# Kernel tuning notes

Measured on AMD Instinct MI355X. Metric: run time of the kernel, lower is better.

## Reference

```python
import jax, jax.numpy as jnp
import numpy as np

HIDDEN = 4096
N_HEADS = 32
N_KV_HEADS = 8
HEAD_DIM = 128
ROPE_THETA = 1e11
KEY_MULTIPLIER = 0.5
Q_SIZE = N_HEADS * HEAD_DIM
KV_SIZE = N_KV_HEADS * HEAD_DIM
SEQ = 2048


def _rope_neox(x, positions):
    # x: [T, H, D]; neox style: rotate halves of the head dim
    d = x.shape[-1]
    inv_freq = 1.0 / (ROPE_THETA ** (jnp.arange(0, d // 2, dtype=jnp.float32) * (2.0 / d)))
    freqs = positions.astype(jnp.float32)[:, None] * inv_freq[None, :]  # [T, D/2]
    cos = jnp.cos(freqs)[:, None, :]  # [T, 1, D/2]
    sin = jnp.sin(freqs)[:, None, :]
    x1, x2 = x[..., : d // 2], x[..., d // 2 :]
    return jnp.concatenate([x1 * cos - x2 * sin, x2 * cos + x1 * sin], axis=-1)


def setup_inputs() -> dict:
    key = jax.random.key(0)
    k1, k2, k3 = jax.random.split(key, 3)
    scale_in = 1.0 / np.sqrt(HIDDEN)
    return {
        "positions": jnp.arange(SEQ, dtype=jnp.int32),
        "hidden_states": jax.random.normal(k1, (SEQ, HIDDEN), jnp.float32),
        "w_qkv": jax.random.normal(k2, (HIDDEN, Q_SIZE + 2 * KV_SIZE), jnp.float32) * scale_in,
        "w_o": jax.random.normal(k3, (Q_SIZE, HIDDEN), jnp.float32) * scale_in,
    }


def reference(positions, hidden_states, w_qkv, w_o):
    T = hidden_states.shape[0]
    qkv = hidden_states @ w_qkv  # [T, q+2kv]
    q, k, v = jnp.split(qkv, [Q_SIZE, Q_SIZE + KV_SIZE], axis=-1)
    k = k * KEY_MULTIPLIER
    q = q.reshape(T, N_HEADS, HEAD_DIM)
    k = k.reshape(T, N_KV_HEADS, HEAD_DIM)
    v = v.reshape(T, N_KV_HEADS, HEAD_DIM)
    q = _rope_neox(q, positions)
    k = _rope_neox(k, positions)
    # GQA: expand kv heads to query heads
    group = N_HEADS // N_KV_HEADS
    k = jnp.repeat(k, group, axis=1)  # [T, H, D]
    v = jnp.repeat(v, group, axis=1)
    scaling = HEAD_DIM ** -0.5
    scores = jnp.einsum("qhd,khd->hqk", q, k) * scaling  # [H, T, T]
    causal = positions[:, None] >= positions[None, :]  # [T, T]
    scores = jnp.where(causal[None, :, :], scores, jnp.finfo(scores.dtype).min)
    probs = jax.nn.softmax(scores, axis=-1)
    attn = jnp.einsum("hqk,khd->qhd", probs, v).reshape(T, Q_SIZE)
    return attn @ w_o
```

## Files before the change

kernel.cpp:

```cpp
#include <hip/hip_runtime.h>
#include <hip/hip_bf16.h>
#include <math.h>

typedef __bf16 bf16_t;
typedef bf16_t bf16x8 __attribute__((ext_vector_type(8)));
typedef bf16_t bf16x4 __attribute__((ext_vector_type(4)));
typedef float  f32x4  __attribute__((ext_vector_type(4)));

#define HIDDEN 4096
#define NH     32
#define NKV    8
#define HD     128
#define QSZ    4096
#define KVSZ   1024
#define QKVN   6144
#define SEQ    2048
#define ATT_SCALE 0.08838834764831845f
#define KEYMUL 0.5f

static __device__ __forceinline__ void gld_lds16(const void* g, void* l) {
  __builtin_amdgcn_global_load_lds((const __attribute__((address_space(1))) char*)g,
                                   (__attribute__((address_space(3))) char*)l, 16, 0, 0);
}

__global__ __launch_bounds__(256) void cast_f32_bf16(const float* __restrict__ in,
                                                     bf16_t* __restrict__ out) {
  int i = (blockIdx.x * 256 + threadIdx.x) * 4;
  float4 v = *(const float4*)(in + i);
  bf16x4 o;
  o[0] = (bf16_t)v.x; o[1] = (bf16_t)v.y; o[2] = (bf16_t)v.z; o[3] = (bf16_t)v.w;
  *(bf16x4*)(out + i) = o;
}

__global__ __launch_bounds__(256) void transpose_cast(const float* __restrict__ W,
                                                      bf16_t* __restrict__ WT,
                                                      int K, int N) {
  __shared__ float t[32][33];
  int k0 = blockIdx.y * 32, n0 = blockIdx.x * 32;
  int c = threadIdx.x & 31, r = threadIdx.x >> 5;
#pragma unroll
  for (int rr = r; rr < 32; rr += 8)
    t[rr][c] = W[(size_t)(k0 + rr) * N + n0 + c];
  __syncthreads();
#pragma unroll
  for (int rr = r; rr < 32; rr += 8)
    WT[(size_t)(n0 + rr) * K + k0 + c] = (bf16_t)t[c][rr];
}

__global__ __launch_bounds__(256) void vprep(const float* __restrict__ qkv,
                                             bf16_t* __restrict__ VT) {
  __shared__ float t[32][33];
  int h = blockIdx.z;
  int s0 = blockIdx.x * 32, d0 = blockIdx.y * 32;
  int c = threadIdx.x & 31, r = threadIdx.x >> 5;
#pragma unroll
  for (int rr = r; rr < 32; rr += 8)
    t[rr][c] = qkv[(size_t)(s0 + rr) * QKVN + QSZ + KVSZ + h * HD + d0 + c];
  __syncthreads();
#pragma unroll
  for (int rr = r; rr < 32; rr += 8)
    VT[((size_t)h * HD + d0 + rr) * SEQ + s0 + c] = (bf16_t)t[c][rr];
}

__global__ __launch_bounds__(256) void rope_qk(const float* __restrict__ qkv,
                                               const int* __restrict__ positions,
                                               bf16_t* __restrict__ Qh,
                                               bf16_t* __restrict__ Kh) {
  int s = blockIdx.x;
  float pos = (float)positions[s];
  for (int p = threadIdx.x; p < (NH + NKV) * 64; p += 256) {
    int i = p & 63;
    float inv = powf(100000000000.0f, -(float)i * (1.0f / 64.0f));
    float fr = pos * inv;
    float cs = cosf(fr), sn = sinf(fr);
    if (p < NH * 64) {
      int hh = p >> 6;
      const float* base = qkv + (size_t)s * QKVN + hh * HD;
      float x1 = base[i], x2 = base[i + 64];
      bf16_t* ob = Qh + ((size_t)hh * SEQ + s) * HD;
      ob[i]      = (bf16_t)(x1 * cs - x2 * sn);
      ob[i + 64] = (bf16_t)(x2 * cs + x1 * sn);
    } else {
      int hh = (p - NH * 64) >> 6;
      const float* base = qkv + (size_t)s * QKVN + QSZ + hh * HD;
      float x1 = base[i], x2 = base[i + 64];
      bf16_t* ob = Kh + ((size_t)hh * SEQ + s) * HD;
      ob[i]      = (bf16_t)((x1 * cs - x2 * sn) * KEYMUL);
      ob[i + 64] = (bf16_t)((x2 * cs + x1 * sn) * KEYMUL);
    }
  }
}

__global__ __launch_bounds__(512, 2) void gemm256(const bf16_t* __restrict__ A,
                                                  const bf16_t* __restrict__ BT,
                                                  float* __restrict__ C,
                                                  int M, int N, int K) {
  __shared__ __align__(16) bf16_t lA[2][256 * 64];
  __shared__ __align__(16) bf16_t lB[2][256 * 64];
  const int tid = threadIdx.x;
  const int w = tid >> 6, lane = tid & 63, l16 = lane & 15, lhi = lane >> 4;
  const int wm2 = w >> 2, wn4 = w & 3;

  const int nbx = N >> 8;
  const int nwg = nbx * (M >> 8);
  int bid = blockIdx.x;
  int swz = (bid & 7) * (nwg >> 3) + (bid >> 3);
  const int bm = swz / nbx, bn = swz % nbx;

  const int NT = K >> 6;

  int sRow[4], sCol[4];
#pragma unroll
  for (int i = 0; i < 4; ++i) {
    int X = i * 8192 + tid * 16;
    sRow[i] = X >> 7;
    sCol[i] = (X & 127) ^ ((sRow[i] & 7) << 4);
  }
  const char* Ag = (const char*)(A + (size_t)bm * 256 * K);
  const char* Bg = (const char*)(BT + (size_t)bn * 256 * K);

  auto stage = [&](int t, int buf) {
#pragma unroll
    for (int i = 0; i < 4; ++i)
      gld_lds16(Ag + (size_t)sRow[i] * (K * 2) + t * 128 + sCol[i],
                (char*)&lA[buf][0] + i * 8192 + tid * 16);
#pragma unroll
    for (int i = 0; i < 4; ++i)
      gld_lds16(Bg + (size_t)sRow[i] * (K * 2) + t * 128 + sCol[i],
                (char*)&lB[buf][0] + i * 8192 + tid * 16);
  };

  f32x4 acc[8][4] = {};
  stage(0, 0);
  stage(1, 1);

  for (int t = 0; t < NT; ++t) {
    const int cur = t & 1;
    if (t == NT - 1) asm volatile("s_waitcnt vmcnt(0)" ::: "memory");
    else             asm volatile("s_waitcnt vmcnt(8)" ::: "memory");
    __builtin_amdgcn_s_barrier();
    asm volatile("" ::: "memory");
    const char* Ab = (const char*)&lA[cur][0];
    const char* Bb = (const char*)&lB[cur][0];

    bf16x8 bF[4][2];
#pragma unroll
    for (int n = 0; n < 4; ++n)
#pragma unroll
      for (int ks = 0; ks < 2; ++ks) {
        int row = wn4 * 64 + n * 16 + l16;
        bF[n][ks] = *(const bf16x8*)(Bb + row * 128 + ((ks * 64 + lhi * 16) ^ ((row & 7) << 4)));
      }
#pragma unroll
    for (int q = 0; q < 4; ++q) {
      bf16x8 aF[2][2];
#pragma unroll
      for (int mi = 0; mi < 2; ++mi)
#pragma unroll
        for (int ks = 0; ks < 2; ++ks) {
          int row = wm2 * 128 + (q * 2 + mi) * 16 + l16;
          aF[mi][ks] = *(const bf16x8*)(Ab + row * 128 + ((ks * 64 + lhi * 16) ^ ((row & 7) << 4)));
        }
      __builtin_amdgcn_s_setprio(1);
#pragma unroll
      for (int mi = 0; mi < 2; ++mi)
#pragma unroll
        for (int n = 0; n < 4; ++n)
#pragma unroll
          for (int ks = 0; ks < 2; ++ks)
            acc[q * 2 + mi][n] = __builtin_amdgcn_mfma_f32_16x16x32_bf16(
                aF[mi][ks], bF[n][ks], acc[q * 2 + mi][n], 0, 0, 0);
      __builtin_amdgcn_s_setprio(0);
    }
    asm volatile("" ::: "memory");
    __builtin_amdgcn_s_barrier();
    asm volatile("" ::: "memory");
    if (t + 2 < NT) stage(t + 2, cur);
  }

#pragma unroll
  for (int m = 0; m < 8; ++m) {
    int row = bm * 256 + wm2 * 128 + m * 16 + lhi * 4;
#pragma unroll
    for (int n = 0; n < 4; ++n) {
      int col = bn * 256 + wn4 * 64 + n * 16 + l16;
#pragma unroll
      for (int j = 0; j < 4; ++j)
        C[(size_t)(row + j) * N + col] = acc[m][n][j];
    }
  }
}

__global__ __launch_bounds__(256) void attn_kernel(const bf16_t* __restrict__ Q,
                                                   const bf16_t* __restrict__ Kb,
                                                   const bf16_t* __restrict__ VT,
                                                   bf16_t* __restrict__ Oa) {
  __shared__ __align__(16) char KV[2][2][16384];
  __shared__ __align__(16) bf16_t Plds[4][16][72];
  int h = blockIdx.y, p = blockIdx.x;
  int kvh = h >> 2;
  int tid = threadIdx.x;
  int w = tid >> 6, lane = tid & 63;
  int l16 = lane & 15, lhi = lane >> 4;
  int xr = (l16 & 7) << 4;

  int kRow[4], kCol[4], vRow[4], vCol[4], ldsOff[4];
#pragma unroll
  for (int i = 0; i < 4; ++i) {
    int X = w * 4096 + i * 1024 + lane * 16;
    ldsOff[i] = X;
    kRow[i] = X >> 8;
    kCol[i] = (X & 255) ^ ((kRow[i] & 7) << 4);
    vRow[i] = X >> 7;
    vCol[i] = (X & 127) ^ ((vRow[i] & 7) << 4);
  }
  const char* Kg = (const char*)(Kb + (size_t)kvh * SEQ * HD);
  const char* Vg = (const char*)(VT + (size_t)kvh * HD * SEQ);

  int qts[2] = {p, 31 - p};
  int nts[2] = {p + 1, 32 - p};

  for (int ph = 0; ph < 2; ++ph) {
    int qt = qts[ph], ntile = nts[ph];
    int qrow0 = qt * 64 + w * 16;

    bf16x8 qf[4];
    const bf16_t* qbase = Q + ((size_t)h * SEQ + qrow0 + l16) * HD;
#pragma unroll
    for (int kk = 0; kk < 4; ++kk)
      qf[kk] = *(const bf16x8*)(qbase + kk * 32 + lhi * 8);

    f32x4 o[8] = {};
    float m_r[4], l_r[4];
#pragma unroll
    for (int j = 0; j < 4; ++j) { m_r[j] = -1e30f; l_r[j] = 0.0f; }

#pragma unroll
    for (int i = 0; i < 4; ++i) {
      gld_lds16(Kg + (size_t)(0 + kRow[i]) * 256 + kCol[i], &KV[0][0][0] + ldsOff[i]);
      gld_lds16(Vg + (size_t)vRow[i] * (SEQ * 2) + 0 + vCol[i], &KV[0][1][0] + ldsOff[i]);
    }
    __syncthreads();

    for (int kt = 0; kt < ntile; ++kt) {
      int b = kt & 1;
      int kb = kt * 64;
      if (kt + 1 < ntile) {
        int kb2 = kb + 64;
#pragma unroll
        for (int i = 0; i < 4; ++i) {
          gld_lds16(Kg + (size_t)(kb2 + kRow[i]) * 256 + kCol[i], &KV[b ^ 1][0][0] + ldsOff[i]);
          gld_lds16(Vg + (size_t)vRow[i] * (SEQ * 2) + (size_t)kb2 * 2 + vCol[i], &KV[b ^ 1][1][0] + ldsOff[i]);
        }
      }
      const char* Kl = &KV[b][0][0];
      const char* Vl = &KV[b][1][0];

      f32x4 s4[4] = {};
#pragma unroll
      for (int n = 0; n < 4; ++n) {
        int r = n * 16 + l16;
#pragma unroll
        for (int kk = 0; kk < 4; ++kk) {
          bf16x8 kf = *(const bf16x8*)(Kl + r * 256 + ((kk * 64 + lhi * 16) ^ xr));
          s4[n] = __builtin_amdgcn_mfma_f32_16x16x32_bf16(qf[kk], kf, s4[n], 0, 0, 0);
        }
      }
      float pv[4][4];
#pragma unroll
      for (int n = 0; n < 4; ++n) {
        int col = kb + n * 16 + l16;
#pragma unroll
        for (int j = 0; j < 4; ++j) {
          int row = qrow0 + lhi * 4 + j;
          float v = s4[n][j] * ATT_SCALE;
          pv[n][j] = (col > row) ? -1e30f : v;
        }
      }
      float mx[4];
#pragma unroll
      for (int j = 0; j < 4; ++j) {
        mx[j] = fmaxf(fmaxf(pv[0][j], pv[1][j]), fmaxf(pv[2][j], pv[3][j]));
#pragma unroll
        for (int d = 1; d < 16; d <<= 1)
          mx[j] = fmaxf(mx[j], __shfl_xor(mx[j], d));
      }
      float mn[4], sc[4], rs[4];
#pragma unroll
      for (int j = 0; j < 4; ++j) {
        mn[j] = fmaxf(m_r[j], mx[j]);
        sc[j] = __expf(m_r[j] - mn[j]);
        m_r[j] = mn[j];
      }
#pragma unroll
      for (int n = 0; n < 4; ++n)
#pragma unroll
        for (int j = 0; j < 4; ++j)
          pv[n][j] = __expf(pv[n][j] - mn[j]);
#pragma unroll
      for (int j = 0; j < 4; ++j) {
        rs[j] = pv[0][j] + pv[1][j] + pv[2][j] + pv[3][j];
#pragma unroll
        for (int d = 1; d < 16; d <<= 1)
          rs[j] += __shfl_xor(rs[j], d);
        l_r[j] = l_r[j] * sc[j] + rs[j];
      }
#pragma unroll
      for (int nf = 0; nf < 8; ++nf)
#pragma unroll
        for (int j = 0; j < 4; ++j)
          o[nf][j] *= sc[j];
#pragma unroll
      for (int n = 0; n < 4; ++n)
#pragma unroll
        for (int j = 0; j < 4; ++j)
          Plds[w][lhi * 4 + j][n * 16 + l16] = (bf16_t)pv[n][j];
#pragma unroll
      for (int ks = 0; ks < 2; ++ks) {
        bf16x8 pa = *(const bf16x8*)&Plds[w][l16][ks * 32 + lhi * 8];
#pragma unroll
        for (int nf = 0; nf < 8; ++nf) {
          int d = nf * 16 + l16;
          bf16x8 vf = *(const bf16x8*)(Vl + d * 128 + ((ks * 64 + lhi * 16) ^ xr));
          o[nf] = __builtin_amdgcn_mfma_f32_16x16x32_bf16(pa, vf, o[nf], 0, 0, 0);
        }
      }
      __syncthreads();
    }
#pragma unroll
    for (int j = 0; j < 4; ++j) {
      float inv_l = 1.0f / l_r[j];
      int row = qrow0 + lhi * 4 + j;
#pragma unroll
      for (int nf = 0; nf < 8; ++nf)
        Oa[(size_t)row * QSZ + h * HD + nf * 16 + l16] = (bf16_t)(o[nf][j] * inv_l);
    }
    __syncthreads();
  }
}

extern "C" void kernel_launch(void* const* d_in, const int* in_sizes, int n_in,
                              void* d_out, int out_size, void* d_ws, size_t ws_size,
                              hipStream_t stream) {
  const int*   positions = (const int*)d_in[0];
  const float* hidden    = (const float*)d_in[1];
  const float* w_qkv     = (const float*)d_in[2];
  const float* w_o       = (const float*)d_in[3];
  float* out = (float*)d_out;

  char* ws = (char*)d_ws;
  size_t off = 0;
  auto alloc = [&](size_t bytes) { void* p = ws + off; off += (bytes + 255) & ~255ULL; return p; };
  bf16_t* h_bf  = (bf16_t*)alloc((size_t)SEQ * HIDDEN * 2);
  bf16_t* wqkvT = (bf16_t*)alloc((size_t)QKVN * HIDDEN * 2);
  bf16_t* woT   = (bf16_t*)alloc((size_t)HIDDEN * QSZ * 2);
  float*  qkv   = (float*)alloc((size_t)SEQ * QKVN * 4);
  bf16_t* Qh    = (bf16_t*)alloc((size_t)NH * SEQ * HD * 2);
  bf16_t* Kh    = (bf16_t*)alloc((size_t)NKV * SEQ * HD * 2);
  bf16_t* VT    = (bf16_t*)alloc((size_t)NKV * HD * SEQ * 2);
  bf16_t* Oa    = (bf16_t*)alloc((size_t)SEQ * QSZ * 2);
  (void)ws_size; (void)in_sizes; (void)n_in; (void)out_size;

  cast_f32_bf16<<<SEQ * HIDDEN / 4 / 256, 256, 0, stream>>>(hidden, h_bf);
  transpose_cast<<<dim3(QKVN / 32, HIDDEN / 32), 256, 0, stream>>>(w_qkv, wqkvT, HIDDEN, QKVN);
  transpose_cast<<<dim3(HIDDEN / 32, QSZ / 32), 256, 0, stream>>>(w_o, woT, QSZ, HIDDEN);
  gemm256<<<(SEQ / 256) * (QKVN / 256), 512, 0, stream>>>(h_bf, wqkvT, qkv, SEQ, QKVN, HIDDEN);
  rope_qk<<<SEQ, 256, 0, stream>>>(qkv, positions, Qh, Kh);
  vprep<<<dim3(SEQ / 32, HD / 32, NKV), 256, 0, stream>>>(qkv, VT);
  attn_kernel<<<dim3(16, NH), 256, 0, stream>>>(Qh, Kh, VT, Oa);
  gemm256<<<(SEQ / 256) * (HIDDEN / 256), 512, 0, stream>>>(Oa, woT, out, SEQ, HIDDEN, QSZ);
}
```

Baseline: 639.5 us.

## Restructure GEMM main loop into quarter-tile ping-pong pipeline with split LDS halves

Splits each 256x64 LDS tile into two 128-row halves and reorganizes the GEMM K-loop into eight barrier-delimited phases per pair of K-steps. Each phase interleaves LDS fragment reads, one half-tile global-to-LDS load, and a 4x2 MFMA block, aiming to hide global load latency and LDS read latency behind matrix math. It adds many extra barriers and relies on precise vmcnt bookkeeping, which risks stalls or hazards, and it assumes an even number of K tiles.

Result: faster. 599.5 us (-6.3%).

```diff
diff --git a/kernel.cpp b/kernel.cpp
--- a/kernel.cpp
+++ b/kernel.cpp
@@ -95,11 +95,12 @@
                                                   const bf16_t* __restrict__ BT,
                                                   float* __restrict__ C,
                                                   int M, int N, int K) {
-  __shared__ __align__(16) bf16_t lA[2][256 * 64];
-  __shared__ __align__(16) bf16_t lB[2][256 * 64];
+  __shared__ __align__(16) bf16_t lA[2][2][128 * 64];
+  __shared__ __align__(16) bf16_t lB[2][2][128 * 64];
   const int tid = threadIdx.x;
   const int w = tid >> 6, lane = tid & 63, l16 = lane & 15, lhi = lane >> 4;
   const int wm2 = w >> 2, wn4 = w & 3;
+  const int xr = (l16 & 7) << 4;
 
   const int nbx = N >> 8;
   const int nwg = nbx * (M >> 8);
@@ -108,74 +109,113 @@
   const int bm = swz / nbx, bn = swz % nbx;
 
   const int NT = K >> 6;
-
-  int sRow[4], sCol[4];
-#pragma unroll
-  for (int i = 0; i < 4; ++i) {
-    int X = i * 8192 + tid * 16;
-    sRow[i] = X >> 7;
-    sCol[i] = (X & 127) ^ ((sRow[i] & 7) << 4);
+  const int NP = NT >> 1;
+
+  int sRow[2], sCol[2];
+#pragma unroll
+  for (int c = 0; c < 2; ++c) {
+    int X = c * 8192 + tid * 16;
+    sRow[c] = X >> 7;
+    sCol[c] = (X & 127) ^ (((X >> 7) & 7) << 4);
   }
   const char* Ag = (const char*)(A + (size_t)bm * 256 * K);
   const char* Bg = (const char*)(BT + (size_t)bn * 256 * K);
 
-  auto stage = [&](int t, int buf) {
-#pragma unroll
-    for (int i = 0; i < 4; ++i)
-      gld_lds16(Ag + (size_t)sRow[i] * (K * 2) + t * 128 + sCol[i],
-                (char*)&lA[buf][0] + i * 8192 + tid * 16);
-#pragma unroll
-    for (int i = 0; i < 4; ++i)
-      gld_lds16(Bg + (size_t)sRow[i] * (K * 2) + t * 128 + sCol[i],
-                (char*)&lB[buf][0] + i * 8192 + tid * 16);
-  };
+  auto stageA = [&](int t, int buf, int h) {
+#pragma unroll
+    for (int c = 0; c < 2; ++c)
+      gld_lds16(Ag + (size_t)(h * 128 + sRow[c]) * (K * 2) + t * 128 + sCol[c],
+                (char*)&lA[buf][h][0] + c * 8192 + tid * 16);
+  };
+  auto stageB = [&](int t, int buf, int h) {
+#pragma unroll
+    for (int c = 0; c < 2; ++c)
+      gld_lds16(Bg + (size_t)(h * 128 + sRow[c]) * (K * 2) + t * 128 + sCol[c],
+                (char*)&lB[buf][h][0] + c * 8192 + tid * 16);
+  };
+
+  const char* AbW[2] = {(const char*)&lA[0][wm2][0], (const char*)&lA[1][wm2][0]};
+  const char* BbW[2] = {(const char*)&lB[0][wn4 >> 1][0], (const char*)&lB[1][wn4 >> 1][0]};
+  const int bRow0 = (wn4 & 1) * 64;
 
   f32x4 acc[8][4] = {};
-  stage(0, 0);
-  stage(1, 1);
-
-  for (int t = 0; t < NT; ++t) {
-    const int cur = t & 1;
-    if (t == NT - 1) asm volatile("s_waitcnt vmcnt(0)" ::: "memory");
-    else             asm volatile("s_waitcnt vmcnt(8)" ::: "memory");
+  bf16x8 aLo[4][2], aHi[4][2], bLo[2][2], bHi[2][2];
+
+  auto rdA = [&](bf16x8 (&dst)[4][2], int buf, int mh) {
+#pragma unroll
+    for (int mi = 0; mi < 4; ++mi)
+#pragma unroll
+      for (int ks = 0; ks < 2; ++ks) {
+        int row = (mh * 4 + mi) * 16 + l16;
+        dst[mi][ks] = *(const bf16x8*)(AbW[buf] + row * 128 + ((ks * 64 + lhi * 16) ^ xr));
+      }
+  };
+  auto rdB = [&](bf16x8 (&dst)[2][2], int buf, int nh) {
+#pragma unroll
+    for (int ni = 0; ni < 2; ++ni)
+#pragma unroll
+      for (int ks = 0; ks < 2; ++ks) {
+        int row = bRow0 + (nh * 2 + ni) * 16 + l16;
+        dst[ni][ks] = *(const bf16x8*)(BbW[buf] + row * 128 + ((ks * 64 + lhi * 16) ^ xr));
+      }
+  };
+  auto doMFMA = [&](bf16x8 (&a)[4][2], bf16x8 (&b)[2][2], int mh, int nh) {
+    __builtin_amdgcn_s_setprio(1);
+#pragma unroll
+    for (int mi = 0; mi < 4; ++mi)
+#pragma unroll
+      for (int ni = 0; ni < 2; ++ni)
+#pragma unroll
+        for (int ks = 0; ks < 2; ++ks)
+          acc[mh * 4 + mi][nh * 2 + ni] = __builtin_amdgcn_mfma_f32_16x16x32_bf16(
+              a[mi][ks], b[ni][ks], acc[mh * 4 + mi][nh * 2 + ni], 0, 0, 0);
+    __builtin_amdgcn_s_setprio(0);
+  };
+  auto openB = [&]() {
+    asm volatile("" ::: "memory");
+    __builtin_amdgcn_s_barrier();
+    asm volatile("s_waitcnt lgkmcnt(0)" ::: "memory");
+    __builtin_amdgcn_sched_barrier(0);
+  };
+  auto closeB = [&](int vm) {
+    asm volatile("" ::: "memory");
+    if (vm == 0)      asm volatile("s_waitcnt vmcnt(0)" ::: "memory");
+    else if (vm > 0)  asm volatile("s_waitcnt vmcnt(4)" ::: "memory");
     __builtin_amdgcn_s_barrier();
     asm volatile("" ::: "memory");
-    const char* Ab = (const char*)&lA[cur][0];
-    const char* Bb = (const char*)&lB[cur][0];
-
-    bf16x8 bF[4][2];
-#pragma unroll
-    for (int n = 0; n < 4; ++n)
-#pragma unroll
-      for (int ks = 0; ks < 2; ++ks) {
-        int row = wn4 * 64 + n * 16 + l16;
-        bF[n][ks] = *(const bf16x8*)(Bb + row * 128 + ((ks * 64 + lhi * 16) ^ ((row & 7) << 4)));
-      }
-#pragma unroll
-    for (int q = 0; q < 4; ++q) {
-      bf16x8 aF[2][2];
-#pragma unroll
-      for (int mi = 0; mi < 2; ++mi)
-#pragma unroll
-        for (int ks = 0; ks < 2; ++ks) {
-          int row = wm2 * 128 + (q * 2 + mi) * 16 + l16;
-          aF[mi][ks] = *(const bf16x8*)(Ab + row * 128 + ((ks * 64 + lhi * 16) ^ ((row & 7) << 4)));
-        }
-      __builtin_amdgcn_s_setprio(1);
-#pragma unroll
-      for (int mi = 0; mi < 2; ++mi)
-#pragma unroll
-        for (int n = 0; n < 4; ++n)
-#pragma unroll
-          for (int ks = 0; ks < 2; ++ks)
-            acc[q * 2 + mi][n] = __builtin_amdgcn_mfma_f32_16x16x32_bf16(
-                aF[mi][ks], bF[n][ks], acc[q * 2 + mi][n], 0, 0, 0);
-      __builtin_amdgcn_s_setprio(0);
-    }
-    asm volatile("" ::: "memory");
-    __builtin_amdgcn_s_barrier();
-    asm volatile("" ::: "memory");
-    if (t + 2 < NT) stage(t + 2, cur);
+  };
+
+  stageA(0, 0, 0); stageA(0, 0, 1); stageB(0, 0, 0); stageB(0, 0, 1);
+  if (NT > 1) { stageB(1, 1, 0); stageB(1, 1, 1); }
+  asm volatile("s_waitcnt vmcnt(4)" ::: "memory");
+  __builtin_amdgcn_s_barrier();
+  asm volatile("" ::: "memory");
+
+  for (int ip = 0; ip < NP; ++ip) {
+    const int t1 = 2 * ip + 1, t2 = 2 * ip + 2, t3 = 2 * ip + 3;
+    const bool s2 = t2 < NT, s3 = t3 < NT;
+    rdB(bLo, 0, 0); rdA(aLo, 0, 0);
+    stageA(t1, 1, 0);
+    openB(); doMFMA(aLo, bLo, 0, 0); closeB(-1);
+    rdB(bHi, 0, 1);
+    stageA(t1, 1, 1);
+    openB(); doMFMA(aLo, bHi, 0, 1); closeB(-1);
+    rdA(aHi, 0, 1);
+    if (s2) stageB(t2, 0, 0);
+    openB(); doMFMA(aHi, bLo, 1, 0); closeB(-1);
+    if (s2) stageB(t2, 0, 1);
+    openB(); doMFMA(aHi, bHi, 1, 1); closeB(s2 ? 4 : 0);
+    rdB(bLo, 1, 0); rdA(aLo, 1, 0);
+    if (s2) stageA(t2, 0, 0);
+    openB(); doMFMA(aLo, bLo, 0, 0); closeB(-1);
+    rdB(bHi, 1, 1);
+    if (s2) stageA(t2, 0, 1);
+    openB(); doMFMA(aLo, bHi, 0, 1); closeB(-1);
+    rdA(aHi, 1, 1);
+    if (s3) stageB(t3, 1, 0);
+    openB(); doMFMA(aHi, bLo, 1, 0); closeB(-1);
+    if (s3) stageB(t3, 1, 1);
+    openB(); doMFMA(aHi, bHi, 1, 1); closeB(4);
   }
 
 #pragma unroll
```
